# Optimization experiments

Hardware: AMD Instinct MI355X
Metric: run time of the kernel (lower is better)

## Reference

```python
import jax, jax.numpy as jnp
import numpy as np

B, S, D = 4, 2048, 1024  # batch, seq_len, input_dim (= dk = dv)


def setup_inputs() -> dict:
    key = jax.random.key(0)
    kx, kq, kk, kv = jax.random.split(key, 4)
    scale = 1.0 / np.sqrt(D)
    return {
        "x": jax.random.normal(kx, (B, S, D), dtype=jnp.float32),
        "Wq": jax.random.normal(kq, (D, D), dtype=jnp.float32) * scale,
        "Wk": jax.random.normal(kk, (D, D), dtype=jnp.float32) * scale,
        "Wv": jax.random.normal(kv, (D, D), dtype=jnp.float32) * scale,
    }


def reference(x, Wq, Wk, Wv):
    # Linear projections (bias=False). W is [in, out].
    Q = jnp.einsum("bsd,de->bse", x, Wq)
    K = jnp.einsum("bsd,de->bse", x, Wk)
    V = jnp.einsum("bsd,de->bse", x, Wv)
    dk = Q.shape[-1]
    # scores: [B, S, S]
    scores = jnp.einsum("bqe,bke->bqk", Q, K) / jnp.sqrt(jnp.float32(dk))
    # causal mask: upper triangle (j > i) masked to -inf
    S_len = x.shape[1]
    causal = jnp.triu(jnp.ones((S_len, S_len), dtype=bool), k=1)
    scores = jnp.where(causal[None, :, :], -jnp.inf, scores)
    attn = jax.nn.softmax(scores, axis=-1)
    # dropout p=0.0 (eval): identity
    return jnp.einsum("bqk,bke->bqe", attn, V)
```

## Files before the change

### kernel.cpp

```cpp
#include <hip/hip_runtime.h>

#define S_LEN 2048
#define DMODEL 1024
#define NBATCH 4

typedef unsigned short u16;
typedef __bf16 bf16x8 __attribute__((ext_vector_type(8)));
typedef float f32x4 __attribute__((ext_vector_type(4)));

typedef __attribute__((address_space(3))) unsigned lds_u32;
typedef const __attribute__((address_space(1))) unsigned glb_u32;

__device__ __forceinline__ u16 f2bf(float f) {
  union { float f; unsigned u; } v;
  v.f = f;
  unsigned r = v.u + 0x7fffu + ((v.u >> 16) & 1u);
  return (u16)(r >> 16);
}

__device__ __forceinline__ float bf2f(u16 h) {
  union { unsigned u; float f; } v;
  v.u = ((unsigned)h) << 16;
  return v.f;
}

#define XCD_SWZ() do { \
    int _nwg = gridDim.x * gridDim.y * gridDim.z; \
    int _hw = blockIdx.x + gridDim.x * (blockIdx.y + gridDim.y * blockIdx.z); \
    int _q = _nwg >> 3; \
    int _w = (_hw & 7) * _q + (_hw >> 3); \
    bm = _w % gridDim.x; _w /= gridDim.x; \
    bn = _w % gridDim.y; bz = _w / gridDim.y; \
  } while (0)

__global__ void convert_x_kernel(const float* __restrict__ x, u16* __restrict__ xb, long n) {
  long i = ((long)blockIdx.x * blockDim.x + threadIdx.x) * 4;
  long stride = (long)gridDim.x * blockDim.x * 4;
  for (; i < n; i += stride) {
    float4 v = *reinterpret_cast<const float4*>(x + i);
    ushort4 o;
    o.x = f2bf(v.x); o.y = f2bf(v.y); o.z = f2bf(v.z); o.w = f2bf(v.w);
    *reinterpret_cast<ushort4*>(xb + i) = o;
  }
}

__global__ void transpose_w3_kernel(const float* __restrict__ Wq, const float* __restrict__ Wk,
                                    const float* __restrict__ Wv, u16* __restrict__ Wt) {
  const float* W = blockIdx.z == 0 ? Wq : (blockIdx.z == 1 ? Wk : Wv);
  u16* dst = Wt + (long)blockIdx.z * 1024 * 1024;
  __shared__ float tile[32][33];
  int tx = threadIdx.x, ty = threadIdx.y;
  int k0 = blockIdx.x * 32, n0 = blockIdx.y * 32;
#pragma unroll
  for (int i = 0; i < 32; i += 8)
    tile[ty + i][tx] = W[(long)(k0 + ty + i) * DMODEL + n0 + tx];
  __syncthreads();
#pragma unroll
  for (int i = 0; i < 32; i += 8)
    dst[(long)(n0 + ty + i) * DMODEL + k0 + tx] = f2bf(tile[tx][ty + i]);
}

#define STG(SRCP, LD, ISB, H, T, BUFB) do { \
    const u16* _s = (SRCP) + (long)(H) * 128 * (LD) + (T) * 64; \
    char* _d = lds + (BUFB) * 65536 + ((ISB) ? 32768 : 0) + ((H) * 8 + w) * 2048; \
    __builtin_amdgcn_global_load_lds((glb_u32*)_s, (lds_u32*)_d, 16, 0, 0); \
    __builtin_amdgcn_global_load_lds((glb_u32*)(_s + 32), (lds_u32*)(_d + 1024), 16, 0, 0); \
  } while (0)

#define READ_A(QM) do { \
    _Pragma("unroll") \
    for (int _i = 0; _i < 4; ++_i) { \
      int _mp = (QM) * 8 + wm * 4 + _i; \
      af[_i][0] = *(const bf16x8*)(_Al + (_mp * 2 + 0) * 1024 + frag_off); \
      af[_i][1] = *(const bf16x8*)(_Al + (_mp * 2 + 1) * 1024 + frag_off); \
    } \
  } while (0)

#define READ_BQ(DST, QN) do { \
    _Pragma("unroll") \
    for (int _j = 0; _j < 2; ++_j) { \
      int _np = (QN) * 8 + wn * 2 + _j; \
      DST[_j][0] = *(const bf16x8*)(_Bl + (_np * 2 + 0) * 1024 + frag_off); \
      DST[_j][1] = *(const bf16x8*)(_Bl + (_np * 2 + 1) * 1024 + frag_off); \
    } \
  } while (0)

#define MFMA16(QM, QN, BREG) do { \
    _Pragma("unroll") \
    for (int _i = 0; _i < 4; ++_i) \
      _Pragma("unroll") \
      for (int _j = 0; _j < 2; ++_j) { \
        acc[QM][QN][_i][_j] = __builtin_amdgcn_mfma_f32_16x16x32_bf16(af[_i][0], BREG[_j][0], acc[QM][QN][_i][_j], 0, 0, 0); \
        acc[QM][QN][_i][_j] = __builtin_amdgcn_mfma_f32_16x16x32_bf16(af[_i][1], BREG[_j][1], acc[QM][QN][_i][_j], 0, 0, 0); \
      } \
  } while (0)

__global__ __launch_bounds__(512, 2) void gemm256_sc(
    const u16* __restrict__ A, const u16* __restrict__ B, u16* __restrict__ Cptr,
    int lda, int ldb, int ldc, int Kdim,
    long sAz, long sBz, long sCz)
{
  int bm, bn, bz;
  XCD_SWZ();
  if (bn > bm) return;
  int NT = Kdim >> 6;

  const u16* Ab = A + (long)bz * sAz + (long)bm * 256 * lda;
  const u16* Bb = B + (long)bz * sBz + (long)bn * 256 * ldb;

  __shared__ char lds[131072];

  int tid = threadIdx.x;
  int lane = tid & 63, w = tid >> 6;
  int wm = w >> 2, wn = w & 3;
  int l15 = lane & 15, lhi = lane >> 4;
  int frag_off = (l15 * 64 + lhi * 16) ^ (((lane >> 3) & 1) << 5);

  int le = lane ^ ((lane >> 5) << 1);
  int lr = le >> 2;
  int kb = (le & 3) * 8;

  const u16* Asrc = Ab + (long)(w * 16 + lr) * lda + kb;
  const u16* Bsrc = Bb + (long)(w * 16 + lr) * ldb + kb;

  f32x4 acc[2][2][4][2];
#pragma unroll
  for (int a = 0; a < 2; ++a)
#pragma unroll
    for (int b = 0; b < 2; ++b)
#pragma unroll
      for (int c = 0; c < 4; ++c)
#pragma unroll
        for (int d = 0; d < 2; ++d)
          acc[a][b][c][d] = (f32x4){0.f, 0.f, 0.f, 0.f};

  STG(Asrc, lda, 0, 0, 0, 0); STG(Bsrc, ldb, 1, 0, 0, 0);
  STG(Asrc, lda, 0, 1, 0, 0); STG(Bsrc, ldb, 1, 1, 0, 0);
  STG(Asrc, lda, 0, 0, 1, 1); STG(Bsrc, ldb, 1, 0, 1, 1);
  asm volatile("s_waitcnt vmcnt(4)" ::: "memory");
  __builtin_amdgcn_s_barrier();

  for (int g = 0; g < NT; ++g) {
    int buf = g & 1;
    int t1 = g + 1; if (t1 >= NT) t1 -= NT;
    int t2 = g + 2; if (t2 >= NT) t2 -= NT;
    const char* _Al = lds + buf * 65536;
    const char* _Bl = _Al + 32768;
    bf16x8 af[4][2], b0[2][2], b1[2][2];

    READ_A(0);
    READ_BQ(b0, 0);
    STG(Asrc, lda, 0, 1, t1, buf ^ 1);
    __builtin_amdgcn_s_barrier();
    asm volatile("s_waitcnt lgkmcnt(0)" ::: "memory");
    __builtin_amdgcn_sched_barrier(0);
    __builtin_amdgcn_s_setprio(1);
    MFMA16(0, 0, b0);
    __builtin_amdgcn_s_setprio(0);
    __builtin_amdgcn_s_barrier();

    READ_BQ(b1, 1);
    STG(Bsrc, ldb, 1, 1, t1, buf ^ 1);
    __builtin_amdgcn_s_barrier();
    asm volatile("s_waitcnt lgkmcnt(0)" ::: "memory");
    __builtin_amdgcn_sched_barrier(0);
    __builtin_amdgcn_s_setprio(1);
    MFMA16(0, 1, b1);
    __builtin_amdgcn_s_setprio(0);
    __builtin_amdgcn_s_barrier();

    READ_A(1);
    STG(Asrc, lda, 0, 0, t2, buf);
    __builtin_amdgcn_s_barrier();
    asm volatile("s_waitcnt lgkmcnt(0)" ::: "memory");
    __builtin_amdgcn_sched_barrier(0);
    __builtin_amdgcn_s_setprio(1);
    MFMA16(1, 1, b1);
    __builtin_amdgcn_s_setprio(0);
    __builtin_amdgcn_s_barrier();

    STG(Bsrc, ldb, 1, 0, t2, buf);
    __builtin_amdgcn_s_barrier();
    __builtin_amdgcn_s_setprio(1);
    MFMA16(1, 0, b0);
    __builtin_amdgcn_s_setprio(0);
    asm volatile("s_waitcnt vmcnt(4)" ::: "memory");
    __builtin_amdgcn_s_barrier();
  }

  int Mbase = bm * 256, Nbase = bn * 256;
  u16* C = Cptr + (long)bz * sCz;
#pragma unroll
  for (int qm = 0; qm < 2; ++qm)
#pragma unroll
    for (int qn = 0; qn < 2; ++qn)
#pragma unroll
      for (int i = 0; i < 4; ++i)
#pragma unroll
        for (int j = 0; j < 2; ++j) {
          int r0 = Mbase + qm * 128 + wm * 64 + i * 16 + lhi * 4;
          int col = Nbase + qn * 128 + wn * 32 + j * 16 + l15;
          f32x4 v = acc[qm][qn][i][j];
#pragma unroll
          for (int r = 0; r < 4; ++r)
            C[(long)(r0 + r) * ldc + col] = f2bf(v[r]);
        }
}

template<int CMODE, int MODE>
__global__ __launch_bounds__(512) void gemm_bk32(
    const u16* __restrict__ A, const u16* __restrict__ B,
    void* __restrict__ Cptr, void* __restrict__ Cptr2,
    int lda, int ldb, int ldc, int Kdim,
    long sAz, long sBz, long sCz)
{
  int bm, bn, bz;
  XCD_SWZ();
  int k0 = 0, Keff = Kdim, h = 0;
  if constexpr (MODE == 4) {
    h = bz & 1;
    bz >>= 1;
    int Klim = (bm + 1) * 128;
    k0 = h * 1024;
    if (k0 >= Klim) return;
    int k1 = k0 + 1024; if (k1 > Klim) k1 = Klim;
    Keff = k1 - k0;
  }
  int NT = Keff >> 5;

  const u16* Ab = A + (long)bz * sAz + (long)bm * 128 * lda + k0;
  const u16* Bb = B + (long)bz * sBz + (long)bn * 256 * ldb + k0;

  __shared__ char lds[73728];

  int tid = threadIdx.x;
  int lane = tid & 63, w = tid >> 6;
  int wm = w >> 2, wn = w & 3;
  int l15 = lane & 15, lhi = lane >> 4;
  int frag_off = (l15 * 64 + lhi * 16) ^ (((lane >> 3) & 1) << 5);

  int le = lane ^ ((lane >> 5) << 1);
  int lr = le >> 2;
  int kb = (le & 3) * 8;

  const u16* Asrc = Ab + (long)(w * 16 + lr) * lda + kb;
  const u16* Bsrc = Bb + (long)(w * 16 + lr) * ldb + kb;

#define STG32(T, BI) do { \
    const u16* _sa = Asrc + (T) * 32; \
    const u16* _sb = Bsrc + (T) * 32; \
    char* _base = lds + (BI) * 24576; \
    __builtin_amdgcn_global_load_lds((glb_u32*)_sa, (lds_u32*)(_base + w * 1024), 16, 0, 0); \
    __builtin_amdgcn_global_load_lds((glb_u32*)_sb, (lds_u32*)(_base + 8192 + w * 1024), 16, 0, 0); \
    __builtin_amdgcn_global_load_lds((glb_u32*)(_sb + (long)128 * ldb), (lds_u32*)(_base + 8192 + (8 + w) * 1024), 16, 0, 0); \
  } while (0)

  f32x4 acc[4][4];
#pragma unroll
  for (int i = 0; i < 4; ++i)
#pragma unroll
    for (int j = 0; j < 4; ++j)
      acc[i][j] = (f32x4){0.f, 0.f, 0.f, 0.f};

  STG32(0, 0);
  STG32(1, 1);
  asm volatile("s_waitcnt vmcnt(3)" ::: "memory");
  __builtin_amdgcn_s_barrier();

  int buf = 0;
  for (int g = 0; g < NT; ++g) {
    bool issue = (g + 2 < NT);
    if (issue) {
      int b2 = buf + 2; if (b2 >= 3) b2 -= 3;
      STG32(g + 2, b2);
    }

    const char* _Al = lds + buf * 24576;
    const char* _Bl = _Al + 8192;
    bf16x8 af[4], bf[4];
#pragma unroll
    for (int i = 0; i < 4; ++i)
      af[i] = *(const bf16x8*)(_Al + (wm * 4 + i) * 1024 + frag_off);
#pragma unroll
    for (int j = 0; j < 4; ++j)
      bf[j] = *(const bf16x8*)(_Bl + (wn * 4 + j) * 1024 + frag_off);

    asm volatile("s_waitcnt lgkmcnt(0)" ::: "memory");
    __builtin_amdgcn_sched_barrier(0);
    __builtin_amdgcn_s_setprio(1);
#pragma unroll
    for (int i = 0; i < 4; ++i)
#pragma unroll
      for (int j = 0; j < 4; ++j)
        acc[i][j] = __builtin_amdgcn_mfma_f32_16x16x32_bf16(af[i], bf[j], acc[i][j], 0, 0, 0);
    __builtin_amdgcn_s_setprio(0);

    if (issue) {
      asm volatile("s_waitcnt vmcnt(3)" ::: "memory");
    } else {
      asm volatile("s_waitcnt vmcnt(0)" ::: "memory");
    }
    __builtin_amdgcn_s_barrier();

    ++buf; if (buf >= 3) buf = 0;
  }
#undef STG32

#pragma unroll
  for (int i = 0; i < 4; ++i)
#pragma unroll
    for (int j = 0; j < 4; ++j) {
      int rl = wm * 64 + i * 16 + lhi * 4;
      int col = bn * 256 + wn * 64 + j * 16 + l15;
      f32x4 v = acc[i][j];
      if constexpr (CMODE == 5) {
        if (h == 0) {
          float* O = (float*)Cptr2 + (long)bz * S_LEN * 1024;
          int row = bm * 128 + rl;
#pragma unroll
          for (int r = 0; r < 4; ++r)
            O[(long)(row + r) * 1024 + col] = v[r];
        } else {
          float* Pp = (float*)Cptr + ((long)((bz * 8 + bm - 8) * 128 + rl)) * 1024 + col;
#pragma unroll
          for (int r = 0; r < 4; ++r)
            Pp[(long)r * 1024] = v[r];
        }
      } else {
        int r0 = bm * 128 + rl;
        if (col < 2048) {
          u16* dst = (u16*)Cptr + (col >= 1024 ? 8388608 : 0);
          int c = col & 1023;
#pragma unroll
          for (int r = 0; r < 4; ++r)
            dst[(long)(r0 + r) * 1024 + c] = f2bf(v[r]);
        } else {
          u16* Vt = (u16*)Cptr + 16777216;
          int e = col - 2048;
          int bb = r0 >> 11, s = r0 & 2047;
          ushort4 u;
          u.x = f2bf(v[0]); u.y = f2bf(v[1]); u.z = f2bf(v[2]); u.w = f2bf(v[3]);
          *reinterpret_cast<ushort4*>(Vt + ((long)bb * 1024 + e) * 2048 + s) = u;
        }
      }
    }
}

__global__ __launch_bounds__(256) void softmax1p(const u16* __restrict__ sc,
                                                 u16* __restrict__ P) {
  int q = blockIdx.x, b = blockIdx.y;
  const u16* srow = sc + ((long)b * S_LEN + q) * S_LEN;
  u16* prow = P + ((long)b * S_LEN + q) * S_LEN;
  int n = q + 1;
  int nz = ((q >> 7) + 1) << 7;
  int tid = threadIdx.x;
  int j0 = tid * 8;
  const float scale = 0.03125f;

  __shared__ float red[8];

  float vs[8];
#pragma unroll
  for (int e = 0; e < 8; ++e) vs[e] = -1e30f;
  if (j0 < n) {
    ushort4 a = *reinterpret_cast<const ushort4*>(srow + j0);
    ushort4 c = *reinterpret_cast<const ushort4*>(srow + j0 + 4);
    vs[0] = bf2f(a.x) * scale; vs[1] = bf2f(a.y) * scale;
    vs[2] = bf2f(a.z) * scale; vs[3] = bf2f(a.w) * scale;
    vs[4] = bf2f(c.x) * scale; vs[5] = bf2f(c.y) * scale;
    vs[6] = bf2f(c.z) * scale; vs[7] = bf2f(c.w) * scale;
#pragma unroll
    for (int e = 0; e < 8; ++e)
      if (j0 + e >= n) vs[e] = -1e30f;
  }

  float m = -1e30f;
#pragma unroll
  for (int e = 0; e < 8; ++e) m = fmaxf(m, vs[e]);
#pragma unroll
  for (int off = 32; off > 0; off >>= 1) m = fmaxf(m, __shfl_xor(m, off, 64));
  if ((tid & 63) == 0) red[tid >> 6] = m;
  __syncthreads();
  float ms = fmaxf(fmaxf(red[0], red[1]), fmaxf(red[2], red[3]));

  float p[8];
  float s = 0.f;
#pragma unroll
  for (int e = 0; e < 8; ++e) { p[e] = __expf(vs[e] - ms); s += (j0 + e < n) ? p[e] : 0.f; }
#pragma unroll
  for (int off = 32; off > 0; off >>= 1) s += __shfl_xor(s, off, 64);
  __syncthreads();
  if ((tid & 63) == 0) red[4 + (tid >> 6)] = s;
  __syncthreads();
  float inv = 1.f / (red[4] + red[5] + red[6] + red[7]);

  if (j0 < nz) {
    ushort4 o0, o1;
    o0.x = (j0 + 0 < n) ? f2bf(p[0] * inv) : (u16)0;
    o0.y = (j0 + 1 < n) ? f2bf(p[1] * inv) : (u16)0;
    o0.z = (j0 + 2 < n) ? f2bf(p[2] * inv) : (u16)0;
    o0.w = (j0 + 3 < n) ? f2bf(p[3] * inv) : (u16)0;
    o1.x = (j0 + 4 < n) ? f2bf(p[4] * inv) : (u16)0;
    o1.y = (j0 + 5 < n) ? f2bf(p[5] * inv) : (u16)0;
    o1.z = (j0 + 6 < n) ? f2bf(p[6] * inv) : (u16)0;
    o1.w = (j0 + 7 < n) ? f2bf(p[7] * inv) : (u16)0;
    *reinterpret_cast<ushort4*>(prow + j0) = o0;
    *reinterpret_cast<ushort4*>(prow + j0 + 4) = o1;
  }
}

__global__ __launch_bounds__(256) void add_pv(const float4* __restrict__ p2,
                                              float4* __restrict__ out) {
  long i = (long)blockIdx.x * 256 + threadIdx.x;
  int c4 = (int)(i & 255);
  long rp = i >> 8;
  int b = (int)(rp >> 10), r = (int)(rp & 1023);
  long oo = ((long)(b * 2048 + 1024 + r) << 8) + c4;
  float4 a = out[oo], d = p2[i];
  a.x += d.x; a.y += d.y; a.z += d.z; a.w += d.w;
  out[oo] = a;
}

extern "C" void kernel_launch(void* const* d_in, const int* in_sizes, int n_in,
                              void* d_out, int out_size, void* d_ws, size_t ws_size,
                              hipStream_t stream) {
  const float* x  = (const float*)d_in[0];
  const float* Wq = (const float*)d_in[1];
  const float* Wk = (const float*)d_in[2];
  const float* Wv = (const float*)d_in[3];
  float* out = (float*)d_out;

  char* ws = (char*)d_ws;
  u16*   xb    = (u16*)(ws);
  u16*   wtb   = (u16*)(ws + 16777216);
  u16*   Qb    = (u16*)(ws + 23068672);
  u16*   Kb    = (u16*)(ws + 39845888);
  u16*   Vtb   = (u16*)(ws + 56623104);
  u16*   scb   = (u16*)(ws + 73400320);
  float* part2 = (float*)(ws + 73400320);
  u16*   P     = (u16*)(ws + 115343360);

  long nx = (long)NBATCH * S_LEN * DMODEL;
  convert_x_kernel<<<2048, 256, 0, stream>>>(x, xb, nx);

  transpose_w3_kernel<<<dim3(32, 32, 3), dim3(32, 8), 0, stream>>>(Wq, Wk, Wv, wtb);

  gemm_bk32<3, 0><<<dim3(64, 12, 1), 512, 0, stream>>>(
      xb, wtb, Qb, nullptr, DMODEL, DMODEL, 0, DMODEL, 0, 0, 0);

  gemm256_sc<<<dim3(8, 8, 4), 512, 0, stream>>>(
      Qb, Kb, scb, DMODEL, DMODEL, S_LEN, DMODEL,
      (long)S_LEN * DMODEL, (long)S_LEN * DMODEL, (long)S_LEN * S_LEN);

  softmax1p<<<dim3(S_LEN, NBATCH), 256, 0, stream>>>(scb, P);

  gemm_bk32<5, 4><<<dim3(16, 4, 8), 512, 0, stream>>>(
      P, Vtb, part2, out, S_LEN, S_LEN, 0, S_LEN,
      (long)S_LEN * S_LEN, (long)DMODEL * S_LEN, 0);

  add_pv<<<4096, 256, 0, stream>>>((const float4*)part2, (float4*)out);
}
```

Measured before the change: 173.7 us.

## Run PV product with 256x256 tiles and drop XCD workgroup swizzle

The attention-times-V product now uses the 256x256 BK64 gemm kernel with split-K halves instead of the 128x256 BK32 kernel. The softmax zero-padding granularity changes from 128 to 256 to match the larger causal tile. The XCD-aware block remapping is removed from all gemm kernels, which now use raw block indices. The aim is more data reuse per tile in the PV product, at the cost of coarser causal tiles that do more wasted work on the diagonal and fewer blocks, and possibly worse L2 locality without the swizzle.

```diff
diff --git a/kernel.cpp b/kernel.cpp
--- a/kernel.cpp
+++ b/kernel.cpp
@@ -23,15 +23,6 @@
   v.u = ((unsigned)h) << 16;
   return v.f;
 }
-
-#define XCD_SWZ() do { \
-    int _nwg = gridDim.x * gridDim.y * gridDim.z; \
-    int _hw = blockIdx.x + gridDim.x * (blockIdx.y + gridDim.y * blockIdx.z); \
-    int _q = _nwg >> 3; \
-    int _w = (_hw & 7) * _q + (_hw >> 3); \
-    bm = _w % gridDim.x; _w /= gridDim.x; \
-    bn = _w % gridDim.y; bz = _w / gridDim.y; \
-  } while (0)
 
 __global__ void convert_x_kernel(const float* __restrict__ x, u16* __restrict__ xb, long n) {
   long i = ((long)blockIdx.x * blockDim.x + threadIdx.x) * 4;
@@ -95,18 +86,34 @@
       } \
   } while (0)
 
-__global__ __launch_bounds__(512, 2) void gemm256_sc(
-    const u16* __restrict__ A, const u16* __restrict__ B, u16* __restrict__ Cptr,
+template<int CMODE, int MODE>
+__global__ __launch_bounds__(512, 2) void gemm256(
+    const u16* __restrict__ A, const u16* __restrict__ B,
+    void* __restrict__ Cptr, void* __restrict__ Cptr2,
     int lda, int ldb, int ldc, int Kdim,
     long sAz, long sBz, long sCz)
 {
-  int bm, bn, bz;
-  XCD_SWZ();
-  if (bn > bm) return;
-  int NT = Kdim >> 6;
-
-  const u16* Ab = A + (long)bz * sAz + (long)bm * 256 * lda;
-  const u16* Bb = B + (long)bz * sBz + (long)bn * 256 * ldb;
+  int bm = blockIdx.x, bn = blockIdx.y, bz = blockIdx.z;
+  int k0 = 0, Keff = Kdim, h = 0;
+  if constexpr (MODE == 1) {
+    if (bn > bm) return;
+  }
+  if constexpr (MODE == 5) {
+    h = bz & 1;
+    bz >>= 1;
+    int Klim = (bm + 1) * 256;
+    if (h == 0) {
+      Keff = Klim < 1024 ? Klim : 1024;
+    } else {
+      if (Klim <= 1024) return;
+      k0 = 1024;
+      Keff = Klim - 1024;
+    }
+  }
+  int NT = Keff >> 6;
+
+  const u16* Ab = A + (long)bz * sAz + (long)bm * 256 * lda + k0;
+  const u16* Bb = B + (long)bz * sBz + (long)bn * 256 * ldb + k0;
 
   __shared__ char lds[131072];
 
@@ -189,7 +196,6 @@
   }
 
   int Mbase = bm * 256, Nbase = bn * 256;
-  u16* C = Cptr + (long)bz * sCz;
 #pragma unroll
   for (int qm = 0; qm < 2; ++qm)
 #pragma unroll
@@ -198,38 +204,41 @@
       for (int i = 0; i < 4; ++i)
 #pragma unroll
         for (int j = 0; j < 2; ++j) {
-          int r0 = Mbase + qm * 128 + wm * 64 + i * 16 + lhi * 4;
+          int rl = qm * 128 + wm * 64 + i * 16 + lhi * 4;
           int col = Nbase + qn * 128 + wn * 32 + j * 16 + l15;
           f32x4 v = acc[qm][qn][i][j];
-#pragma unroll
-          for (int r = 0; r < 4; ++r)
-            C[(long)(r0 + r) * ldc + col] = f2bf(v[r]);
+          if constexpr (CMODE == 1) {
+            u16* C = (u16*)Cptr + (long)bz * sCz;
+            int r0 = Mbase + rl;
+#pragma unroll
+            for (int r = 0; r < 4; ++r)
+              C[(long)(r0 + r) * ldc + col] = f2bf(v[r]);
+          } else {
+            if (h == 0) {
+              float* O = (float*)Cptr2 + (long)bz * S_LEN * 1024;
+              int row = Mbase + rl;
+#pragma unroll
+              for (int r = 0; r < 4; ++r)
+                O[(long)(row + r) * 1024 + col] = v[r];
+            } else {
+              float* Pp = (float*)Cptr + ((long)(bz * 1024 + (bm - 4) * 256 + rl)) * 1024 + col;
+#pragma unroll
+              for (int r = 0; r < 4; ++r)
+                Pp[(long)r * 1024] = v[r];
+            }
+          }
         }
 }
 
-template<int CMODE, int MODE>
-__global__ __launch_bounds__(512) void gemm_bk32(
-    const u16* __restrict__ A, const u16* __restrict__ B,
-    void* __restrict__ Cptr, void* __restrict__ Cptr2,
-    int lda, int ldb, int ldc, int Kdim,
-    long sAz, long sBz, long sCz)
+__global__ __launch_bounds__(512) void gemm_proj(
+    const u16* __restrict__ A, const u16* __restrict__ B, void* __restrict__ Cptr,
+    int lda, int ldb, int Kdim)
 {
-  int bm, bn, bz;
-  XCD_SWZ();
-  int k0 = 0, Keff = Kdim, h = 0;
-  if constexpr (MODE == 4) {
-    h = bz & 1;
-    bz >>= 1;
-    int Klim = (bm + 1) * 128;
-    k0 = h * 1024;
-    if (k0 >= Klim) return;
-    int k1 = k0 + 1024; if (k1 > Klim) k1 = Klim;
-    Keff = k1 - k0;
-  }
-  int NT = Keff >> 5;
-
-  const u16* Ab = A + (long)bz * sAz + (long)bm * 128 * lda + k0;
-  const u16* Bb = B + (long)bz * sBz + (long)bn * 256 * ldb + k0;
+  int bm = blockIdx.x, bn = blockIdx.y;
+  int NT = Kdim >> 5;
+
+  const u16* Ab = A + (long)bm * 128 * lda;
+  const u16* Bb = B + (long)bn * 256 * ldb;
 
   __shared__ char lds[73728];
 
@@ -313,35 +322,20 @@
       int rl = wm * 64 + i * 16 + lhi * 4;
       int col = bn * 256 + wn * 64 + j * 16 + l15;
       f32x4 v = acc[i][j];
-      if constexpr (CMODE == 5) {
-        if (h == 0) {
-          float* O = (float*)Cptr2 + (long)bz * S_LEN * 1024;
-          int row = bm * 128 + rl;
-#pragma unroll
-          for (int r = 0; r < 4; ++r)
-            O[(long)(row + r) * 1024 + col] = v[r];
-        } else {
-          float* Pp = (float*)Cptr + ((long)((bz * 8 + bm - 8) * 128 + rl)) * 1024 + col;
-#pragma unroll
-          for (int r = 0; r < 4; ++r)
-            Pp[(long)r * 1024] = v[r];
-        }
+      int r0 = bm * 128 + rl;
+      if (col < 2048) {
+        u16* dst = (u16*)Cptr + (col >= 1024 ? 8388608 : 0);
+        int c = col & 1023;
+#pragma unroll
+        for (int r = 0; r < 4; ++r)
+          dst[(long)(r0 + r) * 1024 + c] = f2bf(v[r]);
       } else {
-        int r0 = bm * 128 + rl;
-        if (col < 2048) {
-          u16* dst = (u16*)Cptr + (col >= 1024 ? 8388608 : 0);
-          int c = col & 1023;
-#pragma unroll
-          for (int r = 0; r < 4; ++r)
-            dst[(long)(r0 + r) * 1024 + c] = f2bf(v[r]);
-        } else {
-          u16* Vt = (u16*)Cptr + 16777216;
-          int e = col - 2048;
-          int bb = r0 >> 11, s = r0 & 2047;
-          ushort4 u;
-          u.x = f2bf(v[0]); u.y = f2bf(v[1]); u.z = f2bf(v[2]); u.w = f2bf(v[3]);
-          *reinterpret_cast<ushort4*>(Vt + ((long)bb * 1024 + e) * 2048 + s) = u;
-        }
+        u16* Vt = (u16*)Cptr + 16777216;
+        int e = col - 2048;
+        int bb = r0 >> 11, s = r0 & 2047;
+        ushort4 u;
+        u.x = f2bf(v[0]); u.y = f2bf(v[1]); u.z = f2bf(v[2]); u.w = f2bf(v[3]);
+        *reinterpret_cast<ushort4*>(Vt + ((long)bb * 1024 + e) * 2048 + s) = u;
       }
     }
 }
@@ -352,7 +346,7 @@
   const u16* srow = sc + ((long)b * S_LEN + q) * S_LEN;
   u16* prow = P + ((long)b * S_LEN + q) * S_LEN;
   int n = q + 1;
-  int nz = ((q >> 7) + 1) << 7;
+  int nz = ((q >> 8) + 1) << 8;
   int tid = threadIdx.x;
   int j0 = tid * 8;
   const float scale = 0.03125f;
@@ -445,16 +439,15 @@
 
   transpose_w3_kernel<<<dim3(32, 32, 3), dim3(32, 8), 0, stream>>>(Wq, Wk, Wv, wtb);
 
-  gemm_bk32<3, 0><<<dim3(64, 12, 1), 512, 0, stream>>>(
-      xb, wtb, Qb, nullptr, DMODEL, DMODEL, 0, DMODEL, 0, 0, 0);
-
-  gemm256_sc<<<dim3(8, 8, 4), 512, 0, stream>>>(
-      Qb, Kb, scb, DMODEL, DMODEL, S_LEN, DMODEL,
+  gemm_proj<<<dim3(64, 12, 1), 512, 0, stream>>>(xb, wtb, Qb, DMODEL, DMODEL, DMODEL);
+
+  gemm256<1, 1><<<dim3(8, 8, 4), 512, 0, stream>>>(
+      Qb, Kb, scb, nullptr, DMODEL, DMODEL, S_LEN, DMODEL,
       (long)S_LEN * DMODEL, (long)S_LEN * DMODEL, (long)S_LEN * S_LEN);
 
   softmax1p<<<dim3(S_LEN, NBATCH), 256, 0, stream>>>(scb, P);
 
-  gemm_bk32<5, 4><<<dim3(16, 4, 8), 512, 0, stream>>>(
+  gemm256<6, 5><<<dim3(8, 4, 8), 512, 0, stream>>>(
       P, Vtb, part2, out, S_LEN, S_LEN, 0, S_LEN,
       (long)S_LEN * S_LEN, (long)DMODEL * S_LEN, 0);
 
```

Measured after the change: 170.7 us. About the same (-1.7%).
